# Kernel tuning notes

Hardware: AMD Instinct MI355X
Metric: run time of the kernel (lower is better)

The kernel has to match this reference:

```python
import jax, jax.numpy as jnp
import numpy as np

N = 100000
E = 1600000
D_IN = 64
D_HID = 64
D_OUT = 64


def setup_inputs() -> dict:
    key = jax.random.key(0)
    ks = jax.random.split(key, 9)
    x = jax.random.normal(ks[0], (N, D_IN), dtype=jnp.float32)
    edge_index = jax.random.randint(ks[1], (2, E), 0, N, dtype=jnp.int64)
    s1 = 1.0 / np.sqrt(D_IN)
    s2 = 1.0 / np.sqrt(D_HID)
    # PyG SAGEConv: lin_l (applied to aggregated neighbors, has bias), lin_r (root, no bias)
    W1_l = jax.random.uniform(ks[2], (D_HID, D_IN), jnp.float32, -s1, s1)
    b1 = jax.random.uniform(ks[3], (D_HID,), jnp.float32, -s1, s1)
    W1_r = jax.random.uniform(ks[4], (D_HID, D_IN), jnp.float32, -s1, s1)
    W2_l = jax.random.uniform(ks[5], (D_OUT, D_HID), jnp.float32, -s2, s2)
    b2 = jax.random.uniform(ks[6], (D_OUT,), jnp.float32, -s2, s2)
    W2_r = jax.random.uniform(ks[7], (D_OUT, D_HID), jnp.float32, -s2, s2)
    return {"x": x, "edge_index": edge_index, "W1_l": W1_l, "b1": b1, "W1_r": W1_r,
            "W2_l": W2_l, "b2": b2, "W2_r": W2_r}


def _sage_conv(x, src, dst, W_l, b, W_r, n_nodes):
    # mean aggregation of source features at destination nodes
    deg = jax.ops.segment_sum(jnp.ones(src.shape[0], x.dtype), dst, num_segments=n_nodes)
    agg = jax.ops.segment_sum(x[src], dst, num_segments=n_nodes)  # [N, d]
    agg = agg / jnp.maximum(deg, 1.0)[:, None]
    return agg @ W_l.T + b + x @ W_r.T


def reference(x, edge_index, W1_l, b1, W1_r, W2_l, b2, W2_r):
    src, dst = edge_index[0], edge_index[1]
    h = jax.nn.relu(_sage_conv(x, src, dst, W1_l, b1, W1_r, N))
    out = _sage_conv(h, src, dst, W2_l, b2, W2_r, N)
    return out
```

## Files before the change

kernel.cpp:

```cpp
#include <hip/hip_runtime.h>
#include <hip/hip_fp16.h>

#define D 64
#define IDXCAP 448
#define NCH 512
#define MAXB 512
#define RMAX 20

typedef _Float16 f16;
typedef _Float16 f16x8 __attribute__((ext_vector_type(8)));
typedef float f32x4 __attribute__((ext_vector_type(4)));

__device__ __forceinline__ float4 h4_to_f4(uint2 u) {
    float2 fa = __half22float2(__builtin_bit_cast(__half2, u.x));
    float2 fb = __half22float2(__builtin_bit_cast(__half2, u.y));
    return make_float4(fa.x, fa.y, fb.x, fb.y);
}


__global__ __launch_bounds__(256) void p1_count_convert(
        const int* __restrict__ dst, int E, int chunk, int* __restrict__ mat, int bshift,
        const float* __restrict__ x, f16* __restrict__ xh, int n4) {
    __shared__ int h[MAXB];
    for (int i = threadIdx.x; i < MAXB; i += 256) h[i] = 0;
    __syncthreads();
    int k = blockIdx.x;
    int e0 = k * chunk;
    int e1 = min(E, e0 + chunk);
    for (int e = e0 + threadIdx.x; e < e1; e += 256)
        atomicAdd(&h[dst[e] >> bshift], 1);
    __syncthreads();
    for (int b = threadIdx.x; b < MAXB; b += 256)
        mat[b * NCH + k] = h[b];
    int t = blockIdx.x * 256 + threadIdx.x;
    int stride = gridDim.x * 256;
    for (int i = t; i < n4; i += stride) {
        float4 v = ((const float4*)x)[i];
        uint2 o;
        o.x = __builtin_bit_cast(unsigned int, __float22half2_rn(make_float2(v.x, v.y)));
        o.y = __builtin_bit_cast(unsigned int, __float22half2_rn(make_float2(v.z, v.w)));
        ((uint2*)xh)[i] = o;
    }
}

__global__ __launch_bounds__(256) void scan_bt(const int* __restrict__ mat, int* __restrict__ tot) {
    __shared__ int sd[256];
    int b = blockIdx.x;
    int s = 0;
    for (int k = threadIdx.x; k < NCH; k += 256) s += mat[b * NCH + k];
    sd[threadIdx.x] = s; __syncthreads();
    for (int off = 128; off > 0; off >>= 1) {
        if (threadIdx.x < off) sd[threadIdx.x] += sd[threadIdx.x + off];
        __syncthreads();
    }
    if (threadIdx.x == 0) tot[b] = sd[0];
}

__global__ __launch_bounds__(512) void scan_tot(const int* __restrict__ tot, int* __restrict__ bucketBase,
                                                int* __restrict__ rowptr, int nbuck, int N, int E) {
    __shared__ int sc[MAXB];
    int t = threadIdx.x;
    int v = (t < nbuck) ? tot[t] : 0;
    sc[t] = v;
    __syncthreads();
    for (int off = 1; off < MAXB; off <<= 1) {
        int add = (t >= off) ? sc[t - off] : 0;
        __syncthreads();
        sc[t] += add;
        __syncthreads();
    }
    if (t < nbuck) bucketBase[t] = sc[t] - v;
    if (t == 0) { bucketBase[nbuck] = E; rowptr[N] = E; }
}

__global__ __launch_bounds__(256) void scan_col(int* __restrict__ mat, const int* __restrict__ bucketBase) {
    __shared__ int part[256];
    int b = blockIdx.x;
    int base = bucketBase[b];
    int t = threadIdx.x;
    int l0 = mat[b * NCH + 2 * t];
    int l1 = mat[b * NCH + 2 * t + 1];
    int lsum = l0 + l1;
    part[t] = lsum;
    __syncthreads();
    for (int off = 1; off < 256; off <<= 1) {
        int add = (t >= off) ? part[t - off] : 0;
        __syncthreads();
        part[t] += add;
        __syncthreads();
    }
    int excl = base + part[t] - lsum;
    mat[b * NCH + 2 * t] = excl;
    mat[b * NCH + 2 * t + 1] = excl + l0;
}

__global__ __launch_bounds__(256) void p2_scatter(
        const int* __restrict__ src, const int* __restrict__ dst, int E, int chunk,
        const int* __restrict__ mat, int bshift, int2* __restrict__ pairs) {
    __shared__ int cur[MAXB];
    int k = blockIdx.x;
    for (int b = threadIdx.x; b < MAXB; b += 256)
        cur[b] = mat[b * NCH + k];
    __syncthreads();
    int e0 = k * chunk;
    int e1 = min(E, e0 + chunk);
    for (int e = e0 + threadIdx.x; e < e1; e += 256) {
        int d = dst[e], s = src[e];
        int pos = atomicAdd(&cur[d >> bshift], 1);
        pairs[pos] = make_int2(d, s);
    }
}

__global__ __launch_bounds__(256) void p3_build(
        const int2* __restrict__ pairs, const int* __restrict__ bucketBase, int bshift,
        int* __restrict__ rowptr, int* __restrict__ csr, int N) {
    __shared__ int hist[1024];
    __shared__ int cur[1024];
    __shared__ int part[256];
    int b = blockIdx.x;
    int npb = 1 << bshift;
    int nb0 = b << bshift;
    int nn = min(N - nb0, npb);
    int e0 = bucketBase[b], e1 = bucketBase[b + 1];
    int cnt = e1 - e0;
    int t = threadIdx.x;
    for (int i = t; i < npb; i += 256) hist[i] = 0;
    __syncthreads();
    bool reg = (cnt <= 256 * RMAX);
    int2 v[RMAX];
    if (reg) {
        #pragma unroll
        for (int r = 0; r < RMAX; ++r) {
            int e = e0 + r * 256 + t;
            if (e < e1) {
                v[r] = pairs[e];
                atomicAdd(&hist[v[r].x - nb0], 1);
            }
        }
    } else {
        for (int e = e0 + t; e < e1; e += 256)
            atomicAdd(&hist[pairs[e].x - nb0], 1);
    }
    __syncthreads();
    int R = (nn + 255) >> 8;
    int base_i = t * R;
    int lsum = 0;
    for (int r = 0; r < R; ++r) { int i = base_i + r; if (i < nn) lsum += hist[i]; }
    part[t] = lsum;
    __syncthreads();
    for (int off = 1; off < 256; off <<= 1) {
        int add = (t >= off) ? part[t - off] : 0;
        __syncthreads();
        part[t] += add;
        __syncthreads();
    }
    int run = e0 + (part[t] - lsum);
    for (int r = 0; r < R; ++r) {
        int i = base_i + r;
        if (i < nn) {
            int hv = hist[i];
            rowptr[nb0 + i] = run;
            cur[i] = run;
            run += hv;
        }
    }
    __syncthreads();
    if (reg) {
        #pragma unroll
        for (int r = 0; r < RMAX; ++r) {
            int e = e0 + r * 256 + t;
            if (e < e1) {
                int pos = atomicAdd(&cur[v[r].x - nb0], 1);
                csr[pos] = v[r].y;
            }
        }
    } else {
        for (int e = e0 + t; e < e1; e += 256) {
            int2 p = pairs[e];
            int pos = atomicAdd(&cur[p.x - nb0], 1);
            csr[pos] = p.y;
        }
    }
}

#define GATHER_BODY(IP)                                                          \
    for (; j + 16 <= deg; j += 16) {                                             \
        int s0 = (IP)[j + r4];                                                   \
        int s1 = (IP)[j + 4 + r4];                                               \
        int s2 = (IP)[j + 8 + r4];                                               \
        int s3 = (IP)[j + 12 + r4];                                              \
        float4 g0 = h4_to_f4(xh2[(size_t)s0 * 16 + f8]);                         \
        float4 g1 = h4_to_f4(xh2[(size_t)s1 * 16 + f8]);                         \
        float4 g2 = h4_to_f4(xh2[(size_t)s2 * 16 + f8]);                         \
        float4 g3 = h4_to_f4(xh2[(size_t)s3 * 16 + f8]);                         \
        acc.x += (g0.x + g1.x) + (g2.x + g3.x);                                  \
        acc.y += (g0.y + g1.y) + (g2.y + g3.y);                                  \
        acc.z += (g0.z + g1.z) + (g2.z + g3.z);                                  \
        acc.w += (g0.w + g1.w) + (g2.w + g3.w);                                  \
    }                                                                            \
    if (j + 8 <= deg) {                                                          \
        int s0 = (IP)[j + r4];                                                   \
        int s1 = (IP)[j + 4 + r4];                                               \
        float4 g0 = h4_to_f4(xh2[(size_t)s0 * 16 + f8]);                         \
        float4 g1 = h4_to_f4(xh2[(size_t)s1 * 16 + f8]);                         \
        acc.x += g0.x + g1.x; acc.y += g0.y + g1.y;                              \
        acc.z += g0.z + g1.z; acc.w += g0.w + g1.w;                              \
        j += 8;                                                                  \
    }                                                                            \
    for (; j < deg; j += 4) {                                                    \
        int jj = j + r4;                                                         \
        if (jj < deg) {                                                          \
            float4 g = h4_to_f4(xh2[(size_t)(IP)[jj] * 16 + f8]);                \
            acc.x += g.x; acc.y += g.y; acc.z += g.z; acc.w += g.w;              \
        }                                                                        \
    }

template<int RELU, int OUT16>
__global__ __launch_bounds__(512, 4) void sage_mfma(
        const f16* __restrict__ xh, const int* __restrict__ rowptr,
        const int* __restrict__ csr,
        const float* __restrict__ Wl, const float* __restrict__ bias,
        const float* __restrict__ Wr,
        f16* __restrict__ out16, float* __restrict__ out32, int n_nodes) {
    __shared__ __align__(16) f16 sB[16 * 512];
    __shared__ __align__(16) f16 sA[8][16 * 72];
    __shared__ int sIdx[8][IDXCAP];

    for (int u = threadIdx.x; u < 16 * 64; u += blockDim.x) {
        int f = u >> 6;
        int l = u & 63;
        int t = f >> 2, q = f & 3;
        const float* Wsel = (q < 2) ? Wl : Wr;
        int d  = t * 16 + (l & 15);
        int k0 = (q & 1) * 32 + (l >> 4) * 8;
        const float4* wp = (const float4*)(Wsel + d * 64 + k0);
        float4 w0 = wp[0], w1 = wp[1];
        uint4 pk;
        pk.x = __builtin_bit_cast(unsigned int, __float22half2_rn(make_float2(w0.x, w0.y)));
        pk.y = __builtin_bit_cast(unsigned int, __float22half2_rn(make_float2(w0.z, w0.w)));
        pk.z = __builtin_bit_cast(unsigned int, __float22half2_rn(make_float2(w1.x, w1.y)));
        pk.w = __builtin_bit_cast(unsigned int, __float22half2_rn(make_float2(w1.z, w1.w)));
        *(uint4*)&sB[f * 512 + l * 8] = pk;
    }
    __syncthreads();

    const int lane = threadIdx.x & 63;
    const int wid  = threadIdx.x >> 6;
    const int r4   = lane >> 4;
    const int f8   = lane & 15;
    f16* myA = &sA[wid][0];
    int* myIdx = &sIdx[wid][0];

    float bias_t[4];
    #pragma unroll
    for (int t = 0; t < 4; ++t) bias_t[t] = bias[t * 16 + f8];

    const int wavesPerBlock = blockDim.x >> 6;
    const int gwave = blockIdx.x * wavesPerBlock + wid;
    const int nwaves = gridDim.x * wavesPerBlock;
    const uint2* __restrict__ xh2 = (const uint2*)xh;

    for (int nb = gwave * 16; nb < n_nodes; nb += nwaves * 16) {
        int rpl = 0;
        {
            int ii = nb + lane;
            if (lane < 17) rpl = rowptr[ii < n_nodes ? ii : n_nodes];
        }
        int rbase = __builtin_amdgcn_readlane(rpl, 0);
        int rend  = __builtin_amdgcn_readlane(rpl, 16);
        int cnt = rend - rbase;
        bool useLds = (cnt <= IDXCAP);

        if (useLds) {
            for (int c = lane; c < cnt; c += 64)
                myIdx[c] = csr[rbase + c];
        }

        int rn = nb + f8; if (rn >= n_nodes) rn = n_nodes - 1;
        const f16x8* rrow = (const f16x8*)(xh + (size_t)rn * 64);
        f16x8 a2 = rrow[r4];
        f16x8 a3 = rrow[4 + r4];

        #pragma unroll 1
        for (int i = 0; i < 16; ++i) {
            int r0 = __builtin_amdgcn_readlane(rpl, i);
            int r1 = __builtin_amdgcn_readlane(rpl, i + 1);
            int deg = r1 - r0;
            float4 acc = make_float4(0.f, 0.f, 0.f, 0.f);
            int j = 0;
            if (useLds) {
                const int* ip = myIdx + (r0 - rbase);
                GATHER_BODY(ip)
            } else {
                const int* ip = csr + r0;
                GATHER_BODY(ip)
            }
            acc.x += __shfl_xor(acc.x, 16, 64);
            acc.y += __shfl_xor(acc.y, 16, 64);
            acc.z += __shfl_xor(acc.z, 16, 64);
            acc.w += __shfl_xor(acc.w, 16, 64);
            acc.x += __shfl_xor(acc.x, 32, 64);
            acc.y += __shfl_xor(acc.y, 32, 64);
            acc.z += __shfl_xor(acc.z, 32, 64);
            acc.w += __shfl_xor(acc.w, 32, 64);
            float iv = 1.0f / (float)(deg > 0 ? deg : 1);
            if (r4 == (i & 3)) {
                uint2 w;
                w.x = __builtin_bit_cast(unsigned int,
                        __float22half2_rn(make_float2(acc.x * iv, acc.y * iv)));
                w.y = __builtin_bit_cast(unsigned int,
                        __float22half2_rn(make_float2(acc.z * iv, acc.w * iv)));
                *(uint2*)&myA[i * 72 + f8 * 4] = w;
            }
        }

        f16x8 a0 = *(const f16x8*)&myA[f8 * 72 + r4 * 8];
        f16x8 a1 = *(const f16x8*)&myA[f8 * 72 + 32 + r4 * 8];

        #pragma unroll
        for (int t = 0; t < 4; ++t) {
            f32x4 c = {0.f, 0.f, 0.f, 0.f};
            c = __builtin_amdgcn_mfma_f32_16x16x32_f16(a0, *(const f16x8*)&sB[(t*4+0)*512 + lane*8], c, 0, 0, 0);
            c = __builtin_amdgcn_mfma_f32_16x16x32_f16(a1, *(const f16x8*)&sB[(t*4+1)*512 + lane*8], c, 0, 0, 0);
            c = __builtin_amdgcn_mfma_f32_16x16x32_f16(a2, *(const f16x8*)&sB[(t*4+2)*512 + lane*8], c, 0, 0, 0);
            c = __builtin_amdgcn_mfma_f32_16x16x32_f16(a3, *(const f16x8*)&sB[(t*4+3)*512 + lane*8], c, 0, 0, 0);
            #pragma unroll
            for (int rr = 0; rr < 4; ++rr) {
                int n = nb + r4 * 4 + rr;
                if (n < n_nodes) {
                    float v = c[rr] + bias_t[t];
                    if (RELU) v = fmaxf(v, 0.f);
                    if (OUT16) out16[(size_t)n * 64 + t * 16 + f8] = (f16)v;
                    else       out32[(size_t)n * 64 + t * 16 + f8] = v;
                }
            }
        }
    }
}


__global__ void count_rank_convert_kernel(const int* __restrict__ dst, int* __restrict__ counts,
                                          int* __restrict__ rank, int E,
                                          const float* __restrict__ x, f16* __restrict__ xh, int n4) {
    int t = blockIdx.x * blockDim.x + threadIdx.x;
    int stride = gridDim.x * blockDim.x;
    int E4 = E >> 2;
    for (int e4 = t; e4 < E4; e4 += stride) {
        int4 d = ((const int4*)dst)[e4];
        int4 rk;
        rk.x = atomicAdd(&counts[d.x], 1);
        rk.y = atomicAdd(&counts[d.y], 1);
        rk.z = atomicAdd(&counts[d.z], 1);
        rk.w = atomicAdd(&counts[d.w], 1);
        ((int4*)rank)[e4] = rk;
    }
    for (int e = (E & ~3) + t; e < E; e += stride)
        rank[e] = atomicAdd(&counts[dst[e]], 1);
    for (int i = t; i < n4; i += stride) {
        float4 v = ((const float4*)x)[i];
        uint2 o;
        o.x = __builtin_bit_cast(unsigned int, __float22half2_rn(make_float2(v.x, v.y)));
        o.y = __builtin_bit_cast(unsigned int, __float22half2_rn(make_float2(v.z, v.w)));
        ((uint2*)xh)[i] = o;
    }
}

__global__ void scan_block_sums(const int* __restrict__ counts, int* __restrict__ partial, int N4) {
    __shared__ int sd[256];
    int idx = blockIdx.x * 256 + threadIdx.x;
    int s = 0;
    if (idx < N4) {
        int4 v = ((const int4*)counts)[idx];
        s = v.x + v.y + v.z + v.w;
    }
    sd[threadIdx.x] = s; __syncthreads();
    for (int off = 128; off > 0; off >>= 1) {
        if (threadIdx.x < off) sd[threadIdx.x] += sd[threadIdx.x + off];
        __syncthreads();
    }
    if (threadIdx.x == 0) partial[blockIdx.x] = sd[0];
}

__global__ void scan_partials(const int* __restrict__ partial, int* __restrict__ pscan,
                              int* __restrict__ rowptr, int NB, int N, int E) {
    if (threadIdx.x == 0 && blockIdx.x == 0) {
        int s = 0;
        for (int i = 0; i < NB; ++i) { pscan[i] = s; s += partial[i]; }
        rowptr[N] = E;
    }
}

__global__ void scan_final(const int* __restrict__ counts, const int* __restrict__ pscan,
                           int* __restrict__ rowptr, int N4) {
    __shared__ int sc[256];
    int idx = blockIdx.x * 256 + threadIdx.x;
    int4 v = make_int4(0, 0, 0, 0);
    if (idx < N4) v = ((const int4*)counts)[idx];
    int msum = v.x + v.y + v.z + v.w;
    sc[threadIdx.x] = msum; __syncthreads();
    for (int off = 1; off < 256; off <<= 1) {
        int add = (threadIdx.x >= (unsigned)off) ? sc[threadIdx.x - off] : 0;
        __syncthreads();
        sc[threadIdx.x] += add;
        __syncthreads();
    }
    int excl = sc[threadIdx.x] - msum + pscan[blockIdx.x];
    if (idx < N4) {
        int4 r;
        r.x = excl;
        r.y = excl + v.x;
        r.z = r.y + v.y;
        r.w = r.z + v.z;
        ((int4*)rowptr)[idx] = r;
    }
}

__global__ void fill_csr2(const int* __restrict__ src, const int* __restrict__ dst,
                          const int* __restrict__ rowptr, const int* __restrict__ rank,
                          int* __restrict__ csr, int E) {
    int t = blockIdx.x * blockDim.x + threadIdx.x;
    int stride = gridDim.x * blockDim.x;
    int E4 = E >> 2;
    for (int e4 = t; e4 < E4; e4 += stride) {
        int4 d = ((const int4*)dst)[e4];
        int4 rk = ((const int4*)rank)[e4];
        int4 s = ((const int4*)src)[e4];
        csr[rowptr[d.x] + rk.x] = s.x;
        csr[rowptr[d.y] + rk.y] = s.y;
        csr[rowptr[d.z] + rk.z] = s.z;
        csr[rowptr[d.w] + rk.w] = s.w;
    }
    for (int e = (E & ~3) + t; e < E; e += stride)
        csr[rowptr[dst[e]] + rank[e]] = src[e];
}


extern "C" void kernel_launch(void* const* d_in, const int* in_sizes, int n_in,
                              void* d_out, int out_size, void* d_ws, size_t ws_size,
                              hipStream_t stream) {
    const float* x   = (const float*)d_in[0];
    const int*   ei  = (const int*)d_in[1];
    const float* W1l = (const float*)d_in[2];
    const float* b1  = (const float*)d_in[3];
    const float* W1r = (const float*)d_in[4];
    const float* W2l = (const float*)d_in[5];
    const float* b2  = (const float*)d_in[6];
    const float* W2r = (const float*)d_in[7];
    float* out = (float*)d_out;

    const int N = in_sizes[0] / D;
    const int E = in_sizes[1] / 2;
    const int* src = ei;
    const int* dst = ei + E;

    int wavesNeeded = (N + 15) / 16;
    int blocks = (wavesNeeded + 7) / 8;

    int bshift = 0;
    while ((1 << bshift) <= 1024 && ((N + (1 << bshift) - 1) >> bshift) > MAXB) ++bshift;
    bool bok = ((1 << bshift) <= 1024) && (((N + (1 << bshift) - 1) >> bshift) <= MAXB);
    int nbuck = bok ? ((N + (1 << bshift) - 1) >> bshift) : 0;

    {
        size_t off = 0;
        auto alloc = [&](size_t bytes) { size_t r = off; off += (bytes + 511) & ~(size_t)511; return r; };
        size_t o_mat    = alloc((size_t)MAXB * NCH * 4);
        size_t o_tot    = alloc((size_t)MAXB * 4);
        size_t o_bb     = alloc((size_t)(MAXB + 1) * 4);
        size_t o_pairs  = alloc((size_t)E * 8);
        size_t o_rowptr = alloc((size_t)(N + 1) * 4);
        size_t o_csr    = alloc((size_t)E * 4);
        size_t o_xh     = alloc((size_t)N * D * 2);
        size_t o_hh     = alloc((size_t)N * D * 2);

        if (bok && E >= 1 && off <= ws_size) {
            int*  mat    = (int*)((char*)d_ws + o_mat);
            int*  tot    = (int*)((char*)d_ws + o_tot);
            int*  bb     = (int*)((char*)d_ws + o_bb);
            int2* pairs  = (int2*)((char*)d_ws + o_pairs);
            int*  rowptr = (int*)((char*)d_ws + o_rowptr);
            int*  csr    = (int*)((char*)d_ws + o_csr);
            f16*  xh     = (f16*)((char*)d_ws + o_xh);
            f16*  hh     = (f16*)((char*)d_ws + o_hh);

            int chunk = (E + NCH - 1) / NCH;
            p1_count_convert<<<NCH, 256, 0, stream>>>(dst, E, chunk, mat, bshift, x, xh, N * D / 4);
            scan_bt<<<nbuck, 256, 0, stream>>>(mat, tot);
            scan_tot<<<1, 512, 0, stream>>>(tot, bb, rowptr, nbuck, N, E);
            scan_col<<<nbuck, 256, 0, stream>>>(mat, bb);
            p2_scatter<<<NCH, 256, 0, stream>>>(src, dst, E, chunk, mat, bshift, pairs);
            p3_build<<<nbuck, 256, 0, stream>>>(pairs, bb, bshift, rowptr, csr, N);

            sage_mfma<1, 1><<<blocks, 512, 0, stream>>>(xh, rowptr, csr, W1l, b1, W1r, hh, nullptr, N);
            sage_mfma<0, 0><<<blocks, 512, 0, stream>>>(hh, rowptr, csr, W2l, b2, W2r, nullptr, out, N);
            return;
        }
    }

    const int N4 = N / 4;
    const int NB = (N4 + 255) / 256;
    size_t off = 0;
    auto alloc = [&](size_t bytes) { size_t r = off; off += (bytes + 511) & ~(size_t)511; return r; };
    size_t f_counts = alloc((size_t)N * 4);
    size_t f_rowptr = alloc((size_t)(N + 1) * 4);
    size_t f_part   = alloc((size_t)NB * 4);
    size_t f_pscan  = alloc((size_t)NB * 4);
    size_t f_csr    = alloc((size_t)E * 4);
    size_t f_xh     = alloc((size_t)N * D * 2);
    size_t f_hh     = alloc((size_t)N * D * 2);

    int* counts  = (int*)((char*)d_ws + f_counts);
    int* rowptr  = (int*)((char*)d_ws + f_rowptr);
    int* partial = (int*)((char*)d_ws + f_part);
    int* pscan   = (int*)((char*)d_ws + f_pscan);
    int* csr     = (int*)((char*)d_ws + f_csr);
    f16* xh      = (f16*)((char*)d_ws + f_xh);
    f16* hh      = (f16*)((char*)d_ws + f_hh);
    int* rank    = (int*)hh;

    hipMemsetAsync(counts, 0, (size_t)N * 4, stream);
    count_rank_convert_kernel<<<2048, 256, 0, stream>>>(dst, counts, rank, E, x, xh, N * D / 4);
    scan_block_sums<<<NB, 256, 0, stream>>>(counts, partial, N4);
    scan_partials<<<1, 64, 0, stream>>>(partial, pscan, rowptr, NB, N, E);
    scan_final<<<NB, 256, 0, stream>>>(counts, pscan, rowptr, N4);
    fill_csr2<<<2048, 256, 0, stream>>>(src, dst, rowptr, rank, csr, E);

    sage_mfma<1, 1><<<blocks, 512, 0, stream>>>(xh, rowptr, csr, W1l, b1, W1r, hh, nullptr, N);
    sage_mfma<0, 0><<<blocks, 512, 0, stream>>>(hh, rowptr, csr, W2l, b2, W2r, nullptr, out, N);
}
```

Measured before the change: 163.2 us.

## Pack bucket-local dst and src into 32-bit pairs and fuse scan kernels

Scatter pairs now pack the bucket-local destination offset (8 bits) and the source index (24 bits) into one 32-bit word instead of an int2. This halves the pairs traffic written by p2_scatter and read twice by p3_build. The separate scan_tot and scan_col kernels are merged into scan_col2, where each bucket block redundantly scans the bucket totals, which saves one launch. The old int2 path is kept as a fallback when bshift is above 8 or N is 2^24 or more.

```diff
diff --git a/kernel.cpp b/kernel.cpp
--- a/kernel.cpp
+++ b/kernel.cpp
@@ -56,9 +56,11 @@
     if (threadIdx.x == 0) tot[b] = sd[0];
 }
 
-__global__ __launch_bounds__(512) void scan_tot(const int* __restrict__ tot, int* __restrict__ bucketBase,
-                                                int* __restrict__ rowptr, int nbuck, int N, int E) {
+__global__ __launch_bounds__(512) void scan_col2(
+        int* __restrict__ mat, const int* __restrict__ tot, int* __restrict__ bucketBase,
+        int* __restrict__ rowptr, int nbuck, int N, int E) {
     __shared__ int sc[MAXB];
+    int b = blockIdx.x;
     int t = threadIdx.x;
     int v = (t < nbuck) ? tot[t] : 0;
     sc[t] = v;
@@ -69,34 +71,25 @@
         sc[t] += add;
         __syncthreads();
     }
-    if (t < nbuck) bucketBase[t] = sc[t] - v;
-    if (t == 0) { bucketBase[nbuck] = E; rowptr[N] = E; }
-}
-
-__global__ __launch_bounds__(256) void scan_col(int* __restrict__ mat, const int* __restrict__ bucketBase) {
-    __shared__ int part[256];
-    int b = blockIdx.x;
-    int base = bucketBase[b];
-    int t = threadIdx.x;
-    int l0 = mat[b * NCH + 2 * t];
-    int l1 = mat[b * NCH + 2 * t + 1];
-    int lsum = l0 + l1;
-    part[t] = lsum;
-    __syncthreads();
-    for (int off = 1; off < 256; off <<= 1) {
-        int add = (t >= off) ? part[t - off] : 0;
-        __syncthreads();
-        part[t] += add;
-        __syncthreads();
-    }
-    int excl = base + part[t] - lsum;
-    mat[b * NCH + 2 * t] = excl;
-    mat[b * NCH + 2 * t + 1] = excl + l0;
-}
-
-__global__ __launch_bounds__(256) void p2_scatter(
+    int base = sc[b] - tot[b];
+    if (t == 0) bucketBase[b] = base;
+    if (b == 0 && t == 0) { bucketBase[nbuck] = E; rowptr[N] = E; }
+    __syncthreads();
+    int l = mat[b * NCH + t];
+    sc[t] = l;
+    __syncthreads();
+    for (int off = 1; off < MAXB; off <<= 1) {
+        int add = (t >= off) ? sc[t - off] : 0;
+        __syncthreads();
+        sc[t] += add;
+        __syncthreads();
+    }
+    mat[b * NCH + t] = base + sc[t] - l;
+}
+
+__global__ __launch_bounds__(256) void p2_scatter_p(
         const int* __restrict__ src, const int* __restrict__ dst, int E, int chunk,
-        const int* __restrict__ mat, int bshift, int2* __restrict__ pairs) {
+        const int* __restrict__ mat, int bshift, unsigned int* __restrict__ pairs) {
     __shared__ int cur[MAXB];
     int k = blockIdx.x;
     for (int b = threadIdx.x; b < MAXB; b += 256)
@@ -104,15 +97,16 @@
     __syncthreads();
     int e0 = k * chunk;
     int e1 = min(E, e0 + chunk);
+    unsigned int lmask = (1u << bshift) - 1u;
     for (int e = e0 + threadIdx.x; e < e1; e += 256) {
         int d = dst[e], s = src[e];
         int pos = atomicAdd(&cur[d >> bshift], 1);
-        pairs[pos] = make_int2(d, s);
-    }
-}
-
-__global__ __launch_bounds__(256) void p3_build(
-        const int2* __restrict__ pairs, const int* __restrict__ bucketBase, int bshift,
+        pairs[pos] = (((unsigned int)d & lmask) << 24) | (unsigned int)s;
+    }
+}
+
+__global__ __launch_bounds__(256) void p3_build_p(
+        const unsigned int* __restrict__ pairs, const int* __restrict__ bucketBase, int bshift,
         int* __restrict__ rowptr, int* __restrict__ csr, int N) {
     __shared__ int hist[1024];
     __shared__ int cur[1024];
@@ -127,19 +121,19 @@
     for (int i = t; i < npb; i += 256) hist[i] = 0;
     __syncthreads();
     bool reg = (cnt <= 256 * RMAX);
-    int2 v[RMAX];
+    unsigned int v[RMAX];
     if (reg) {
         #pragma unroll
         for (int r = 0; r < RMAX; ++r) {
             int e = e0 + r * 256 + t;
             if (e < e1) {
                 v[r] = pairs[e];
-                atomicAdd(&hist[v[r].x - nb0], 1);
+                atomicAdd(&hist[v[r] >> 24], 1);
             }
         }
     } else {
         for (int e = e0 + t; e < e1; e += 256)
-            atomicAdd(&hist[pairs[e].x - nb0], 1);
+            atomicAdd(&hist[pairs[e] >> 24], 1);
     }
     __syncthreads();
     int R = (nn + 255) >> 8;
@@ -170,16 +164,80 @@
         for (int r = 0; r < RMAX; ++r) {
             int e = e0 + r * 256 + t;
             if (e < e1) {
-                int pos = atomicAdd(&cur[v[r].x - nb0], 1);
-                csr[pos] = v[r].y;
+                int pos = atomicAdd(&cur[v[r] >> 24], 1);
+                csr[pos] = (int)(v[r] & 0xFFFFFFu);
             }
         }
     } else {
         for (int e = e0 + t; e < e1; e += 256) {
-            int2 p = pairs[e];
-            int pos = atomicAdd(&cur[p.x - nb0], 1);
-            csr[pos] = p.y;
-        }
+            unsigned int p = pairs[e];
+            int pos = atomicAdd(&cur[p >> 24], 1);
+            csr[pos] = (int)(p & 0xFFFFFFu);
+        }
+    }
+}
+
+__global__ __launch_bounds__(256) void p2_scatter(
+        const int* __restrict__ src, const int* __restrict__ dst, int E, int chunk,
+        const int* __restrict__ mat, int bshift, int2* __restrict__ pairs) {
+    __shared__ int cur[MAXB];
+    int k = blockIdx.x;
+    for (int b = threadIdx.x; b < MAXB; b += 256)
+        cur[b] = mat[b * NCH + k];
+    __syncthreads();
+    int e0 = k * chunk;
+    int e1 = min(E, e0 + chunk);
+    for (int e = e0 + threadIdx.x; e < e1; e += 256) {
+        int d = dst[e], s = src[e];
+        int pos = atomicAdd(&cur[d >> bshift], 1);
+        pairs[pos] = make_int2(d, s);
+    }
+}
+
+__global__ __launch_bounds__(256) void p3_build(
+        const int2* __restrict__ pairs, const int* __restrict__ bucketBase, int bshift,
+        int* __restrict__ rowptr, int* __restrict__ csr, int N) {
+    __shared__ int hist[1024];
+    __shared__ int cur[1024];
+    __shared__ int part[256];
+    int b = blockIdx.x;
+    int npb = 1 << bshift;
+    int nb0 = b << bshift;
+    int nn = min(N - nb0, npb);
+    int e0 = bucketBase[b], e1 = bucketBase[b + 1];
+    int t = threadIdx.x;
+    for (int i = t; i < npb; i += 256) hist[i] = 0;
+    __syncthreads();
+    for (int e = e0 + t; e < e1; e += 256)
+        atomicAdd(&hist[pairs[e].x - nb0], 1);
+    __syncthreads();
+    int R = (nn + 255) >> 8;
+    int base_i = t * R;
+    int lsum = 0;
+    for (int r = 0; r < R; ++r) { int i = base_i + r; if (i < nn) lsum += hist[i]; }
+    part[t] = lsum;
+    __syncthreads();
+    for (int off = 1; off < 256; off <<= 1) {
+        int add = (t >= off) ? part[t - off] : 0;
+        __syncthreads();
+        part[t] += add;
+        __syncthreads();
+    }
+    int run = e0 + (part[t] - lsum);
+    for (int r = 0; r < R; ++r) {
+        int i = base_i + r;
+        if (i < nn) {
+            int hv = hist[i];
+            rowptr[nb0 + i] = run;
+            cur[i] = run;
+            run += hv;
+        }
+    }
+    __syncthreads();
+    for (int e = e0 + t; e < e1; e += 256) {
+        int2 p = pairs[e];
+        int pos = atomicAdd(&cur[p.x - nb0], 1);
+        csr[pos] = p.y;
     }
 }
 
@@ -460,6 +518,7 @@
     while ((1 << bshift) <= 1024 && ((N + (1 << bshift) - 1) >> bshift) > MAXB) ++bshift;
     bool bok = ((1 << bshift) <= 1024) && (((N + (1 << bshift) - 1) >> bshift) <= MAXB);
     int nbuck = bok ? ((N + (1 << bshift) - 1) >> bshift) : 0;
+    bool packed = bok && (bshift <= 8) && (N < (1 << 24));
 
     {
         size_t off = 0;
@@ -477,7 +536,7 @@
             int*  mat    = (int*)((char*)d_ws + o_mat);
             int*  tot    = (int*)((char*)d_ws + o_tot);
             int*  bb     = (int*)((char*)d_ws + o_bb);
-            int2* pairs  = (int2*)((char*)d_ws + o_pairs);
+            void* pairs  = (void*)((char*)d_ws + o_pairs);
             int*  rowptr = (int*)((char*)d_ws + o_rowptr);
             int*  csr    = (int*)((char*)d_ws + o_csr);
             f16*  xh     = (f16*)((char*)d_ws + o_xh);
@@ -486,10 +545,14 @@
             int chunk = (E + NCH - 1) / NCH;
             p1_count_convert<<<NCH, 256, 0, stream>>>(dst, E, chunk, mat, bshift, x, xh, N * D / 4);
             scan_bt<<<nbuck, 256, 0, stream>>>(mat, tot);
-            scan_tot<<<1, 512, 0, stream>>>(tot, bb, rowptr, nbuck, N, E);
-            scan_col<<<nbuck, 256, 0, stream>>>(mat, bb);
-            p2_scatter<<<NCH, 256, 0, stream>>>(src, dst, E, chunk, mat, bshift, pairs);
-            p3_build<<<nbuck, 256, 0, stream>>>(pairs, bb, bshift, rowptr, csr, N);
+            scan_col2<<<nbuck, 512, 0, stream>>>(mat, tot, bb, rowptr, nbuck, N, E);
+            if (packed) {
+                p2_scatter_p<<<NCH, 256, 0, stream>>>(src, dst, E, chunk, mat, bshift, (unsigned int*)pairs);
+                p3_build_p<<<nbuck, 256, 0, stream>>>((const unsigned int*)pairs, bb, bshift, rowptr, csr, N);
+            } else {
+                p2_scatter<<<NCH, 256, 0, stream>>>(src, dst, E, chunk, mat, bshift, (int2*)pairs);
+                p3_build<<<nbuck, 256, 0, stream>>>((const int2*)pairs, bb, bshift, rowptr, csr, N);
+            }
 
             sage_mfma<1, 1><<<blocks, 512, 0, stream>>>(xh, rowptr, csr, W1l, b1, W1r, hh, nullptr, N);
             sage_mfma<0, 0><<<blocks, 512, 0, stream>>>(hh, rowptr, csr, W2l, b2, W2r, nullptr, out, N);
```

After: 161.6 us. About the same (-1.0%).
